# Kernel tuning notes

Hardware: AMD Instinct MI355X
Metric: run time of the kernel (lower is better)

The kernel has to match this reference:

```python
import jax, jax.numpy as jnp
import numpy as np
from jax.scipy.special import i0

# torchkbnufft default configuration
N = 256          # image size per dim (im_size)
OSF = 2          # grid oversampling factor (default grid_size = 2*im_size)
G = N * OSF      # oversampled grid size = 512
W = 6            # kernel width (numpoints default)
ALPHA = 2.34 * W # Kaiser-Bessel shape parameter (kbwidth default 2.34)
M = 65536        # number of non-uniform k-space samples
B, C = 2, 8      # batch, coils


def _kb_ft(t):
    """Analytic Fourier transform of the KB kernel (for deapodization)."""
    s2 = ALPHA ** 2 - (jnp.pi * W * t) ** 2
    z = jnp.sqrt(jnp.abs(s2)) + 1e-12
    return jnp.where(s2 >= 0, jnp.sinh(z) / z, jnp.sin(z) / z)


def _kb(d):
    """Kaiser-Bessel interpolation kernel, d = distance in grid units."""
    u = 1.0 - (2.0 * d / W) ** 2
    return jnp.where(u > 0, i0(ALPHA * jnp.sqrt(jnp.maximum(u, 1e-12))), 0.0) / W


def setup_inputs() -> dict:
    key = jax.random.key(0)
    k1, k2 = jax.random.split(key)
    x_image = jax.random.normal(k1, (B, C, N, N), dtype=jnp.float32)
    # trajectory in radians/sample, uniform in [-pi, pi)
    k_traj = (jax.random.uniform(k2, (2, M), dtype=jnp.float32) - 0.5) * (2 * jnp.pi)
    return {"x_image": x_image, "k_traj": k_traj}


def reference(x_image, k_traj):
    # 1) deapodization (scaling coefficients), centered image convention
    n = jnp.arange(N, dtype=jnp.float32) - N / 2
    sc = 1.0 / _kb_ft(n / G)                       # (N,)
    xs = (x_image * (sc[:, None] * sc[None, :])).astype(jnp.complex64)

    # 2) zero-pad onto oversampled grid with image centered at index 0 (mod G)
    grid = jnp.zeros(x_image.shape[:2] + (G, G), jnp.complex64)
    grid = grid.at[..., :N, :N].set(xs)
    grid = jnp.roll(grid, shift=(-(N // 2), -(N // 2)), axis=(-2, -1))
    Xk = jnp.fft.fft2(grid)                        # (B,C,G,G) uniform k-space

    # 3) KB interpolation onto non-uniform points (irregular gather)
    tm = k_traj * (G / (2 * jnp.pi))               # continuous grid coords, (2,M)
    offs = jnp.arange(-(W // 2) + 1, W // 2 + 1, dtype=jnp.float32)  # [-2..3]
    base = jnp.floor(tm)
    pts = base[:, :, None] + offs                  # (2,M,W) neighbor coords
    wts = _kb(tm[:, :, None] - pts)                # (2,M,W) real weights
    idx = pts.astype(jnp.int32) % G                # wrap (periodic grid)

    gathered = Xk[:, :, idx[0][:, :, None], idx[1][:, None, :]]  # (B,C,M,W,W)
    y = jnp.einsum('bcmij,mi,mj->bcm', gathered,
                   wts[0].astype(jnp.complex64), wts[1].astype(jnp.complex64))
    # return complex result as stacked (real, imag) float32 for the harness
    return jnp.stack([y.real, y.imag], axis=-1)   # (B,C,M,2)
```

## Files before the change

kernel.cpp:

```cpp
#include <hip/hip_runtime.h>
#include <hip/hip_fp16.h>
#include <math.h>

#define NN 256
#define GSZ 512
#define GG (GSZ * GSZ)
#define BC 16
#define MM 65536
#define ALPHA_C 14.04f
#define WKER 6
#define PI_F 3.14159265358979f
#define RC2 0.70710678118654752f
#define KSCALE 81.48733086305042f

#define SSCALE 16777216.0f
#define INV_SSCALE 5.9604644775390625e-8f

#define CAP 144
#define TRW 21
#define TPITCH 23
#define PLANE (TRW * TPITCH)
#define QPL 8
#define NPQ (QPL * TRW * TRW)

__device__ __forceinline__ __half2* regA(float2* grid, int bc) {
    return (__half2*)((char*)grid + (size_t)bc * ((size_t)GG * 8));
}
__device__ __forceinline__ const __half2* regA_c(const float2* grid, int bc) {
    return (const __half2*)((const char*)grid + (size_t)bc * ((size_t)GG * 8));
}
__device__ __forceinline__ __half2* gh_plane(float2* grid, int bc) {
    return (__half2*)((char*)grid + (size_t)bc * ((size_t)GG * 8) + 524288);
}
__device__ __forceinline__ const __half2* gh_plane_c(const float2* grid, int bc) {
    return (const __half2*)((const char*)grid + (size_t)bc * ((size_t)GG * 8) + 524288);
}


__device__ __forceinline__ float bessel_i0(float x) {
    if (x < 3.75f) {
        float t = x * (1.0f / 3.75f);
        float t2 = t * t;
        return 1.0f + t2 * (3.5156229f + t2 * (3.0899424f + t2 * (1.2067492f +
                     t2 * (0.2659732f + t2 * (0.0360768f + t2 * 0.0045813f)))));
    } else {
        float t = 3.75f / x;
        float p = 0.39894228f + t * (0.01328592f + t * (0.00225319f + t * (-0.00157565f +
                  t * (0.00916281f + t * (-0.02057706f + t * (0.02635537f +
                  t * (-0.01647633f + t * 0.00392377f)))))));
        return p * __expf(x) * rsqrtf(x);
    }
}

__device__ __forceinline__ float kb_weight(float d) {
    float r = d * (2.0f / (float)WKER);
    float u = 1.0f - r * r;
    if (u <= 0.0f) return 0.0f;
    return bessel_i0(ALPHA_C * sqrtf(u)) * (1.0f / (float)WKER);
}

__device__ __forceinline__ float kb_ft_inv(float t) {
    float a = PI_F * (float)WKER * t;
    float s2 = ALPHA_C * ALPHA_C - a * a;
    float z = sqrtf(fabsf(s2)) + 1e-12f;
    float sh = 0.5f * (__expf(z) - __expf(-z));
    return z / sh;
}

__device__ __forceinline__ void cmul(float& zr, float& zi, float wr, float wi) {
    float r = zr * wr - zi * wi;
    zi = zr * wi + zi * wr;
    zr = r;
}


template <int L>
__device__ __forceinline__ void radix8_stage(float* pr, float* pi_, int j) {
    int pos = j & (L - 1);
    int base = (j - pos) * 8 + pos;
    float ar[8], ai[8];
#pragma unroll
    for (int r = 0; r < 8; ++r) {
        int idx = base + r * L;
        int ph = idx + (idx >> 3);
        ar[r] = pr[ph];
        ai[r] = pi_[ph];
    }
    if (L > 1) {
        float th = (float)pos * (-PI_F / (4.0f * (float)L));
        float s1, c1;
        __sincosf(th, &s1, &c1);
        float wr = c1, wi = s1;
#pragma unroll
        for (int r = 1; r < 8; ++r) {
            cmul(ar[r], ai[r], wr, wi);
            float nr = wr * c1 - wi * s1;
            wi = wr * s1 + wi * c1;
            wr = nr;
        }
    }
    float s0r = ar[0] + ar[4], s0i = ai[0] + ai[4];
    float d0r = ar[0] - ar[4], d0i = ai[0] - ai[4];
    float s1r = ar[2] + ar[6], s1i = ai[2] + ai[6];
    float d1r = ar[2] - ar[6], d1i = ai[2] - ai[6];
    float E0r = s0r + s1r, E0i = s0i + s1i;
    float E2r = s0r - s1r, E2i = s0i - s1i;
    float E1r = d0r + d1i, E1i = d0i - d1r;
    float E3r = d0r - d1i, E3i = d0i + d1r;
    float u0r = ar[1] + ar[5], u0i = ai[1] + ai[5];
    float v0r = ar[1] - ar[5], v0i = ai[1] - ai[5];
    float u1r = ar[3] + ar[7], u1i = ai[3] + ai[7];
    float v1r = ar[3] - ar[7], v1i = ai[3] - ai[7];
    float O0r = u0r + u1r, O0i = u0i + u1i;
    float O2r = u0r - u1r, O2i = u0i - u1i;
    float O1r = v0r + v1i, O1i = v0i - v1r;
    float O3r = v0r - v1i, O3i = v0i + v1r;
    float t1r = RC2 * (O1r + O1i), t1i = RC2 * (O1i - O1r);
    float t2r = O2i,               t2i = -O2r;
    float t3r = RC2 * (O3i - O3r), t3i = -RC2 * (O3r + O3i);
    float xr[8], xi[8];
    xr[0] = E0r + O0r; xi[0] = E0i + O0i;
    xr[4] = E0r - O0r; xi[4] = E0i - O0i;
    xr[1] = E1r + t1r; xi[1] = E1i + t1i;
    xr[5] = E1r - t1r; xi[5] = E1i - t1i;
    xr[2] = E2r + t2r; xi[2] = E2i + t2i;
    xr[6] = E2r - t2r; xi[6] = E2i - t2i;
    xr[3] = E3r + t3r; xi[3] = E3i + t3i;
    xr[7] = E3r - t3r; xi[7] = E3i - t3i;
#pragma unroll
    for (int q = 0; q < 8; ++q) {
        int idx = base + q * L;
        int ph = idx + (idx >> 3);
        pr[ph] = xr[q];
        pi_[ph] = xi[q];
    }
}


#define LDSP 576
#define ROWBLK (BC * 64)
__global__ void __launch_bounds__(256) k_fft_row_bin(
    const float* __restrict__ x, float2* __restrict__ grid,
    const float* __restrict__ kt, unsigned* __restrict__ cnt,
    unsigned* __restrict__ meta, __half2* __restrict__ whalf) {
    __shared__ float re[4][LDSP], im[4][LDSP];
    int b = blockIdx.x;
    int t = threadIdx.x;
    if (b >= ROWBLK) {
        int m = (b - ROWBLK) * 256 + t;
        float tmx = kt[m] * KSCALE;
        float tmy = kt[MM + m] * KSCALE;
        float bx = floorf(tmx), by = floorf(tmy);
        int ibx = (int)bx & (GSZ - 1);
        int iby = (int)by & (GSZ - 1);
        int tile = ((ibx >> 4) << 5) | (iby >> 4);
        unsigned slot = atomicAdd(&cnt[tile], 1u);
        if (slot < CAP) {
            int idx = tile * CAP + (int)slot;
            int lx = ibx & 15;
            int ly = iby & 15;
            meta[idx] = ((unsigned)m << 8) | (unsigned)(lx << 4) | (unsigned)ly;
            float w0[6], w1[6];
#pragma unroll
            for (int o = 0; o < 6; ++o) {
                float offv = (float)(o - 2);
                w0[o] = kb_weight(tmx - (bx + offv));
                w1[o] = kb_weight(tmy - (by + offv));
            }
            __half2* wp = whalf + (size_t)idx * 6;
            wp[0] = __half2(__float2half_rn(w0[0]), __float2half_rn(w0[1]));
            wp[1] = __half2(__float2half_rn(w0[2]), __float2half_rn(w0[3]));
            wp[2] = __half2(__float2half_rn(w0[4]), __float2half_rn(w0[5]));
            wp[3] = __half2(__float2half_rn(w1[0]), __float2half_rn(w1[1]));
            wp[4] = __half2(__float2half_rn(w1[2]), __float2half_rn(w1[3]));
            wp[5] = __half2(__float2half_rn(w1[4]), __float2half_rn(w1[5]));
        }
        return;
    }
    int w = t >> 6;
    int l = t & 63;
    int rg = (b & 63) * 4 + w;
    int bc = b >> 6;
    int r = (rg < 128) ? rg : rg + 256;
    int r_img = rg ^ 128;
    float scx = kb_ft_inv((float)(r_img - 128) * (1.0f / (float)GSZ));
    const float* xrow = x + ((size_t)bc * NN + (size_t)r_img) * NN;
#pragma unroll
    for (int e = 0; e < 8; ++e) {
        int i = e * 64 + l;
        float v = 0.0f;
        if (i < 128 || i >= 384) {
            int y = (i + 128) & (GSZ - 1);
            float scy = kb_ft_inv((float)(y - 128) * (1.0f / (float)GSZ));
            v = xrow[y] * scx * scy;
        }
        int rev = (l & 7) * 64 + (l >> 3) * 8 + e;
        int ph = rev + (rev >> 3);
        re[w][ph] = v;
        im[w][ph] = 0.0f;
    }
    __syncthreads();
    radix8_stage<1>(re[w], im[w], l);
    __syncthreads();
    radix8_stage<8>(re[w], im[w], l);
    __syncthreads();
    radix8_stage<64>(re[w], im[w], l);
    __syncthreads();
    __half2* pa = regA(grid, bc);
    int slot = (r < 128) ? r : r - 256;
    size_t abase = (size_t)slot * GSZ;
#pragma unroll
    for (int e = 0; e < 8; ++e) {
        int k = e * 64 + l;
        int ph = k + (k >> 3);
        pa[abase + k] = __float22half2_rn(
            make_float2(re[w][ph] * SSCALE, im[w][ph] * SSCALE));
    }
}


#define CSTR 577
__global__ void __launch_bounds__(512) k_fft_col(float2* __restrict__ grid) {
    __shared__ float re[16][CSTR], im[16][CSTR];
    int b = blockIdx.x;
    int bc = b >> 5;
    int c0 = (b & 31) << 4;
    const __half2* pa = regA_c(grid, bc);
    int t = threadIdx.x;
#pragma unroll
    for (int it = 0; it < 16; ++it) {
        int idx = it * 512 + t;
        int row = idx >> 4, col = idx & 15;
        float2 v = make_float2(0.0f, 0.0f);
        if (row < 128)
            v = __half22float2(pa[(size_t)row * GSZ + c0 + col]);
        else if (row >= 384)
            v = __half22float2(pa[(size_t)(row - 256) * GSZ + c0 + col]);
        int rev = (row & 7) * 64 + ((row >> 3) & 7) * 8 + (row >> 6);
        int ph = rev + (rev >> 3);
        re[col][ph] = v.x;
        im[col][ph] = v.y;
    }
    __syncthreads();
    int col = t & 15, jg = t >> 4;
#pragma unroll
    for (int k = 0; k < 2; ++k) radix8_stage<1>(re[col], im[col], jg + 32 * k);
    __syncthreads();
#pragma unroll
    for (int k = 0; k < 2; ++k) radix8_stage<8>(re[col], im[col], jg + 32 * k);
    __syncthreads();
#pragma unroll
    for (int k = 0; k < 2; ++k) radix8_stage<64>(re[col], im[col], jg + 32 * k);
    __syncthreads();
    __half2* ghp = gh_plane(grid, bc);
#pragma unroll
    for (int it = 0; it < 16; ++it) {
        int idx = it * 512 + t;
        int row = idx >> 4, c = idx & 15;
        int ph = row + (row >> 3);
        ghp[(size_t)row * GSZ + c0 + c] =
            __float22half2_rn(make_float2(re[c][ph], im[c][ph]));
    }
}


__global__ void __launch_bounds__(128, 6) k_gather_tile(
    const float2* __restrict__ grid, const unsigned* __restrict__ cnt,
    const unsigned* __restrict__ meta, const __half2* __restrict__ whalf,
    float2* __restrict__ out) {
    __shared__ __half2 ldsh[QPL * PLANE];
    int bid = blockIdx.x;
    int b = ((bid & 7) << 8) | (bid >> 3);
    int tile = b >> 1;
    int oct = b & 1;
    int bc0 = oct * QPL;
    int tx0 = (tile >> 5) << 4;
    int ty0 = (tile & 31) << 4;
    int t = threadIdx.x;
#pragma unroll
    for (int k = 0; k < 28; ++k) {
        int idx = t + (k << 7);
        if (idx < NPQ) {
            int p = idx / (TRW * TRW);
            int rem = idx - p * (TRW * TRW);
            int r = rem / TRW;
            int c = rem - r * TRW;
            int row = (tx0 - 2 + r) & (GSZ - 1);
            int col = (ty0 - 2 + c) & (GSZ - 1);
            ldsh[p * PLANE + r * TPITCH + c] =
                gh_plane_c(grid, bc0 + p)[(size_t)row * GSZ + col];
        }
    }
    int n = (int)cnt[tile];
    if (n > CAP) n = CAP;
    __syncthreads();
    int g = t >> 6;
    int base0 = (4 * g) * PLANE;
    int base1 = base0 + PLANE;
    int base2 = base1 + PLANE;
    int base3 = base2 + PLANE;
    int bcw = bc0 + 4 * g;
    for (int s = (t & 63); s < n; s += 64) {
        int idx = tile * CAP + s;
        unsigned mc = meta[idx];
        int m = (int)(mc >> 8);
        int lx = (int)((mc >> 4) & 15u);
        int ly = (int)(mc & 15u);
        const __half2* wp = whalf + (size_t)idx * 6;
        __half2 p0 = wp[0], p1 = wp[1], p2 = wp[2];
        __half2 q0 = wp[3], q1 = wp[4], q2 = wp[5];
        float w0v[6], w1v[6];
        w0v[0] = __low2float(p0) * INV_SSCALE;
        w0v[1] = __high2float(p0) * INV_SSCALE;
        w0v[2] = __low2float(p1) * INV_SSCALE;
        w0v[3] = __high2float(p1) * INV_SSCALE;
        w0v[4] = __low2float(p2) * INV_SSCALE;
        w0v[5] = __high2float(p2) * INV_SSCALE;
        w1v[0] = __low2float(q0);
        w1v[1] = __high2float(q0);
        w1v[2] = __low2float(q1);
        w1v[3] = __high2float(q1);
        w1v[4] = __low2float(q2);
        w1v[5] = __high2float(q2);
        int off0 = lx * TPITCH + ly;
        float ar0 = 0.f, ai0 = 0.f, ar1 = 0.f, ai1 = 0.f;
        float ar2 = 0.f, ai2 = 0.f, ar3 = 0.f, ai3 = 0.f;
#pragma unroll
        for (int ii = 0; ii < 6; ++ii) {
            float wi = w0v[ii];
            int rowoff = off0 + ii * TPITCH;
#pragma unroll
            for (int j = 0; j < 6; ++j) {
                float wv = wi * w1v[j];
                int o = rowoff + j;
                float2 v0 = __half22float2(ldsh[base0 + o]);
                float2 v1 = __half22float2(ldsh[base1 + o]);
                float2 v2 = __half22float2(ldsh[base2 + o]);
                float2 v3 = __half22float2(ldsh[base3 + o]);
                ar0 = fmaf(wv, v0.x, ar0);
                ai0 = fmaf(wv, v0.y, ai0);
                ar1 = fmaf(wv, v1.x, ar1);
                ai1 = fmaf(wv, v1.y, ai1);
                ar2 = fmaf(wv, v2.x, ar2);
                ai2 = fmaf(wv, v2.y, ai2);
                ar3 = fmaf(wv, v3.x, ar3);
                ai3 = fmaf(wv, v3.y, ai3);
            }
        }
        out[(size_t)(bcw + 0) * MM + m] = make_float2(ar0, ai0);
        out[(size_t)(bcw + 1) * MM + m] = make_float2(ar1, ai1);
        out[(size_t)(bcw + 2) * MM + m] = make_float2(ar2, ai2);
        out[(size_t)(bcw + 3) * MM + m] = make_float2(ar3, ai3);
    }
}

__global__ void k_gather(const float2* __restrict__ grid, const float* __restrict__ kt,
                         float2* __restrict__ out) {
    int tid = blockIdx.x * blockDim.x + threadIdx.x;
    int m = tid & (MM - 1);
    int bc = tid >> 16;
    float tmx = kt[m] * KSCALE;
    float tmy = kt[MM + m] * KSCALE;
    float bx = floorf(tmx), by = floorf(tmy);
    int ibx = (int)bx, iby = (int)by;
    float w0[6], w1[6];
    int ix[6], iy[6];
#pragma unroll
    for (int o = 0; o < 6; ++o) {
        float offv = (float)(o - 2);
        w0[o] = kb_weight(tmx - (bx + offv)) * INV_SSCALE;
        w1[o] = kb_weight(tmy - (by + offv));
        ix[o] = (ibx + (o - 2) + GSZ) & (GSZ - 1);
        iy[o] = (iby + (o - 2) + GSZ) & (GSZ - 1);
    }
    const __half2* img = gh_plane_c(grid, bc);
    float ar = 0.0f, ai = 0.0f;
#pragma unroll
    for (int i = 0; i < 6; ++i) {
        const __half2* rowp = img + (size_t)ix[i] * GSZ;
        float wi = w0[i];
#pragma unroll
        for (int j = 0; j < 6; ++j) {
            float2 v = __half22float2(rowp[iy[j]]);
            float wv = wi * w1[j];
            ar = fmaf(wv, v.x, ar);
            ai = fmaf(wv, v.y, ai);
        }
    }
    out[(size_t)bc * MM + m] = make_float2(ar, ai);
}

__global__ void __launch_bounds__(256) k_fft_row(const float* __restrict__ x,
                                                 float2* __restrict__ grid) {
    __shared__ float re[4][LDSP], im[4][LDSP];
    int b = blockIdx.x;
    int t = threadIdx.x;
    int w = t >> 6;
    int l = t & 63;
    int rg = (b & 63) * 4 + w;
    int bc = b >> 6;
    int r = (rg < 128) ? rg : rg + 256;
    int r_img = rg ^ 128;
    float scx = kb_ft_inv((float)(r_img - 128) * (1.0f / (float)GSZ));
    const float* xrow = x + ((size_t)bc * NN + (size_t)r_img) * NN;
#pragma unroll
    for (int e = 0; e < 8; ++e) {
        int i = e * 64 + l;
        float v = 0.0f;
        if (i < 128 || i >= 384) {
            int y = (i + 128) & (GSZ - 1);
            float scy = kb_ft_inv((float)(y - 128) * (1.0f / (float)GSZ));
            v = xrow[y] * scx * scy;
        }
        int rev = (l & 7) * 64 + (l >> 3) * 8 + e;
        int ph = rev + (rev >> 3);
        re[w][ph] = v;
        im[w][ph] = 0.0f;
    }
    __syncthreads();
    radix8_stage<1>(re[w], im[w], l);
    __syncthreads();
    radix8_stage<8>(re[w], im[w], l);
    __syncthreads();
    radix8_stage<64>(re[w], im[w], l);
    __syncthreads();
    __half2* pa = regA(grid, bc);
    int slot = (r < 128) ? r : r - 256;
    size_t abase = (size_t)slot * GSZ;
#pragma unroll
    for (int e = 0; e < 8; ++e) {
        int k = e * 64 + l;
        int ph = k + (k >> 3);
        pa[abase + k] = __float22half2_rn(
            make_float2(re[w][ph] * SSCALE, im[w][ph] * SSCALE));
    }
}


extern "C" void kernel_launch(void* const* d_in, const int* in_sizes, int n_in,
                              void* d_out, int out_size, void* d_ws, size_t ws_size,
                              hipStream_t stream) {
    const float* x = (const float*)d_in[0];
    const float* kt = (const float*)d_in[1];
    float2* out = (float2*)d_out;
    char* ws = (char*)d_ws;

    const size_t GRID_BYTES = (size_t)BC * GG * sizeof(float2);
    const size_t CNT_BYTES = 1024 * sizeof(unsigned);
    const size_t META_BYTES = (size_t)1024 * CAP * sizeof(unsigned);
    const size_t WH_BYTES = (size_t)1024 * CAP * 6 * sizeof(__half2);
    float2* grid = (float2*)ws;
    unsigned* cnt = (unsigned*)(ws + GRID_BYTES);
    unsigned* meta = (unsigned*)(ws + GRID_BYTES + CNT_BYTES);
    __half2* whalf = (__half2*)(ws + GRID_BYTES + CNT_BYTES + META_BYTES);
    const size_t NEED = GRID_BYTES + CNT_BYTES + META_BYTES + WH_BYTES;

    if (ws_size >= NEED) {
        hipMemsetAsync(cnt, 0, CNT_BYTES, stream);
        k_fft_row_bin<<<ROWBLK + 256, 256, 0, stream>>>(x, grid, kt, cnt, meta, whalf);
        k_fft_col<<<BC * (GSZ / 16), 512, 0, stream>>>(grid);
        k_gather_tile<<<2048, 128, 0, stream>>>(grid, cnt, meta, whalf, out);
    } else {
        k_fft_row<<<BC * 64, 256, 0, stream>>>(x, grid);
        k_fft_col<<<BC * (GSZ / 16), 512, 0, stream>>>(grid);
        k_gather<<<(BC * MM) / 256, 256, 0, stream>>>(grid, kt, out);
    }
}
```

Baseline: 66.29 us.

## Use packed half2 FMA with paired LDS layout in tile gather kernel

```diff
diff --git a/kernel.cpp b/kernel.cpp
--- a/kernel.cpp
+++ b/kernel.cpp
@@ -18,10 +18,9 @@
 
 #define CAP 144
 #define TRW 21
-#define TPITCH 23
-#define PLANE (TRW * TPITCH)
 #define QPL 8
-#define NPQ (QPL * TRW * TRW)
+#define RPW 13
+#define PLW (TRW * RPW)
 
 __device__ __forceinline__ __half2* regA(float2* grid, int bc) {
     return (__half2*)((char*)grid + (size_t)bc * ((size_t)GG * 8));
@@ -34,6 +33,10 @@
 }
 __device__ __forceinline__ const __half2* gh_plane_c(const float2* grid, int bc) {
     return (const __half2*)((const char*)grid + (size_t)bc * ((size_t)GG * 8) + 524288);
+}
+
+__device__ __forceinline__ __half2 u2h(unsigned u) {
+    union { unsigned u; __half2 h; } x; x.u = u; return x.h;
 }
 
 
@@ -264,11 +267,11 @@
 }
 
 
-__global__ void __launch_bounds__(128, 6) k_gather_tile(
+__global__ void __launch_bounds__(128, 4) k_gather_tile(
     const float2* __restrict__ grid, const unsigned* __restrict__ cnt,
     const unsigned* __restrict__ meta, const __half2* __restrict__ whalf,
     float2* __restrict__ out) {
-    __shared__ __half2 ldsh[QPL * PLANE];
+    __shared__ uint2 ldsq[QPL * PLW];
     int bid = blockIdx.x;
     int b = ((bid & 7) << 8) | (bid >> 3);
     int tile = b >> 1;
@@ -278,27 +281,25 @@
     int ty0 = (tile & 31) << 4;
     int t = threadIdx.x;
 #pragma unroll
-    for (int k = 0; k < 28; ++k) {
+    for (int k = 0; k < 15; ++k) {
         int idx = t + (k << 7);
-        if (idx < NPQ) {
-            int p = idx / (TRW * TRW);
-            int rem = idx - p * (TRW * TRW);
-            int r = rem / TRW;
-            int c = rem - r * TRW;
-            int row = (tx0 - 2 + r) & (GSZ - 1);
-            int col = (ty0 - 2 + c) & (GSZ - 1);
-            ldsh[p * PLANE + r * TPITCH + c] =
-                gh_plane_c(grid, bc0 + p)[(size_t)row * GSZ + col];
+        if (idx < QPL * TRW * 11) {
+            int p = idx / (TRW * 11);
+            int rem = idx - p * (TRW * 11);
+            int r = rem / 11;
+            int c = rem - r * 11;
+            int grow = (tx0 - 2 + r) & (GSZ - 1);
+            int gcol = (ty0 - 2 + 2 * c) & (GSZ - 1);
+            const __half2* gp = gh_plane_c(grid, bc0 + p);
+            ldsq[p * PLW + r * RPW + c] =
+                *(const uint2*)(gp + (size_t)grow * GSZ + gcol);
         }
     }
     int n = (int)cnt[tile];
     if (n > CAP) n = CAP;
     __syncthreads();
     int g = t >> 6;
-    int base0 = (4 * g) * PLANE;
-    int base1 = base0 + PLANE;
-    int base2 = base1 + PLANE;
-    int base3 = base2 + PLANE;
+    int pb0 = (4 * g) * PLW;
     int bcw = bc0 + 4 * g;
     for (int s = (t & 63); s < n; s += 64) {
         int idx = tile * CAP + s;
@@ -322,29 +323,46 @@
         w1v[3] = __high2float(q1);
         w1v[4] = __low2float(q2);
         w1v[5] = __high2float(q2);
-        int off0 = lx * TPITCH + ly;
+        bool par = (ly & 1) != 0;
+        int qb = pb0 + lx * RPW + (ly >> 1);
         float ar0 = 0.f, ai0 = 0.f, ar1 = 0.f, ai1 = 0.f;
         float ar2 = 0.f, ai2 = 0.f, ar3 = 0.f, ai3 = 0.f;
 #pragma unroll
         for (int ii = 0; ii < 6; ++ii) {
             float wi = w0v[ii];
-            int rowoff = off0 + ii * TPITCH;
-#pragma unroll
-            for (int j = 0; j < 6; ++j) {
-                float wv = wi * w1v[j];
-                int o = rowoff + j;
-                float2 v0 = __half22float2(ldsh[base0 + o]);
-                float2 v1 = __half22float2(ldsh[base1 + o]);
-                float2 v2 = __half22float2(ldsh[base2 + o]);
-                float2 v3 = __half22float2(ldsh[base3 + o]);
-                ar0 = fmaf(wv, v0.x, ar0);
-                ai0 = fmaf(wv, v0.y, ai0);
-                ar1 = fmaf(wv, v1.x, ar1);
-                ai1 = fmaf(wv, v1.y, ai1);
-                ar2 = fmaf(wv, v2.x, ar2);
-                ai2 = fmaf(wv, v2.y, ai2);
-                ar3 = fmaf(wv, v3.x, ar3);
-                ai3 = fmaf(wv, v3.y, ai3);
+            float wv0 = wi * w1v[0], wv1 = wi * w1v[1], wv2 = wi * w1v[2];
+            float wv3 = wi * w1v[3], wv4 = wi * w1v[4], wv5 = wi * w1v[5];
+            float sl0 = par ? 0.f : wv0;
+            float sl1 = par ? wv0 : wv1;
+            float sl2 = par ? wv1 : wv2;
+            float sl3 = par ? wv2 : wv3;
+            float sl4 = par ? wv3 : wv4;
+            float sl5 = par ? wv4 : wv5;
+            float sl6 = par ? wv5 : 0.f;
+            __half2 h0 = __float22half2_rn(make_float2(sl0, sl0));
+            __half2 h1 = __float22half2_rn(make_float2(sl1, sl1));
+            __half2 h2 = __float22half2_rn(make_float2(sl2, sl2));
+            __half2 h3 = __float22half2_rn(make_float2(sl3, sl3));
+            __half2 h4 = __float22half2_rn(make_float2(sl4, sl4));
+            __half2 h5 = __float22half2_rn(make_float2(sl5, sl5));
+            __half2 h6 = __float22half2_rn(make_float2(sl6, sl6));
+            int qr = qb + ii * RPW;
+#pragma unroll
+            for (int pp = 0; pp < 4; ++pp) {
+                const uint2* lq = &ldsq[qr + pp * PLW];
+                uint2 d0 = lq[0], d1 = lq[1], d2 = lq[2], d3 = lq[3];
+                __half2 acc = __hmul2(h0, u2h(d0.x));
+                acc = __hfma2(h1, u2h(d0.y), acc);
+                acc = __hfma2(h2, u2h(d1.x), acc);
+                acc = __hfma2(h3, u2h(d1.y), acc);
+                acc = __hfma2(h4, u2h(d2.x), acc);
+                acc = __hfma2(h5, u2h(d2.y), acc);
+                acc = __hfma2(h6, u2h(d3.x), acc);
+                float2 f = __half22float2(acc);
+                if (pp == 0) { ar0 += f.x; ai0 += f.y; }
+                else if (pp == 1) { ar1 += f.x; ai1 += f.y; }
+                else if (pp == 2) { ar2 += f.x; ai2 += f.y; }
+                else { ar3 += f.x; ai3 += f.y; }
             }
         }
         out[(size_t)(bcw + 0) * MM + m] = make_float2(ar0, ai0);
```

New measurement: 66.98 us. Within noise of the previous version (+1.0%).
